# Performance work log

Measured on AMD Instinct MI355X. Metric: run time of the kernel, lower is better.

Reference implementation:

```python
import jax, jax.numpy as jnp
import numpy as np

NUM_HEADS = 16
BASE = 10000.0


def setup_inputs() -> dict:
    key = jax.random.key(0)
    ks = jax.random.split(key, 5)
    b, n, c = 4, 4096, 1024
    return {
        "x": jax.random.normal(ks[0], (b, n, c), jnp.float32),
        "W_qk": jax.random.normal(ks[1], (2 * c, c), jnp.float32) * 0.02,
        "b_qk": jax.random.normal(ks[2], (2 * c,), jnp.float32) * 0.02,
        "lepe_w": jax.random.normal(ks[3], (c, 1, 3), jnp.float32) * 0.1,
        "lepe_b": jax.random.normal(ks[4], (c,), jnp.float32) * 0.02,
    }


def _rope(t, cos_t, sin_t):
    # t: (b, n, c); pairs rotated by per-pair angle theta_k (constant over positions,
    # faithful to the original module's RoPE which has no position dependence)
    k_max = t.shape[-1] // 2
    tr = t.reshape(*t.shape[:-1], k_max, 2)
    x0, x1 = tr[..., 0], tr[..., 1]
    out = jnp.stack([cos_t * x0 - sin_t * x1, sin_t * x0 + cos_t * x1], axis=-1)
    return out.reshape(t.shape)


def reference(x, W_qk, b_qk, lepe_w, lepe_b):
    b, n, c = x.shape
    h = NUM_HEADS
    d = c // h
    k_max = c // 2
    theta = 1.0 / (BASE ** (jnp.arange(k_max, dtype=jnp.float32) / k_max))
    cos_t, sin_t = jnp.cos(theta), jnp.sin(theta)

    qk = x @ W_qk.T + b_qk                      # (b, n, 2c)
    q = jax.nn.elu(qk[..., :c]) + 1.0           # (b, n, c)
    k = jax.nn.elu(qk[..., c:]) + 1.0

    q_rope = _rope(q, cos_t, sin_t).reshape(b, n, h, d).transpose(0, 2, 1, 3)
    k_rope = _rope(k, cos_t, sin_t).reshape(b, n, h, d).transpose(0, 2, 1, 3)
    qh = q.reshape(b, n, h, d).transpose(0, 2, 1, 3)
    kh = k.reshape(b, n, h, d).transpose(0, 2, 1, 3)
    vh = x.reshape(b, n, h, d).transpose(0, 2, 1, 3)

    # z normalization: q . mean_n(k)
    z = 1.0 / (jnp.einsum("bhnd,bhd->bhn", qh, kh.mean(axis=2)) + 1e-6)  # (b,h,n)

    # kv accumulation: (k_rope / sqrt(n))^T @ (v / sqrt(n))  -> (b,h,d,d)
    kv = jnp.einsum("bhnd,bhne->bhde", k_rope, vh) * (1.0 / n)
    attn = jnp.einsum("bhnd,bhde->bhne", q_rope, kv) * z[..., None]  # (b,h,n,d)
    out = attn.transpose(0, 2, 1, 3).reshape(b, n, c)

    # depthwise conv positional term on v (== x, since v is x reshaped back)
    v_cn = x.transpose(0, 2, 1)  # (b, c, n)
    pe = jax.lax.conv_general_dilated(
        v_cn, lepe_w, window_strides=(1,), padding=((1, 1),),
        feature_group_count=c, dimension_numbers=("NCH", "OIH", "NCH"))
    pe = pe + lepe_b[None, :, None]
    return out + pe.transpose(0, 2, 1)
```

## Files before the change

### kernel.cpp

```cpp
#include <hip/hip_runtime.h>
#include <hip/hip_bf16.h>
#include <math.h>

typedef unsigned short u16;
typedef __attribute__((ext_vector_type(8))) short s16x8;
typedef __attribute__((ext_vector_type(4))) float f32x4;

#define B_ 4
#define N_ 4096
#define C_ 1024
#define M_ (B_*N_)
#define NT_ 16

__device__ __forceinline__ u16 f2bf(float f) {
  unsigned u = __builtin_bit_cast(unsigned, f);
  u = u + 0x7fffu + ((u >> 16) & 1u);
  return (u16)(u >> 16);
}
__device__ __forceinline__ float bf2f(u16 h) {
  unsigned u = ((unsigned)h) << 16;
  return __builtin_bit_cast(float, u);
}

__global__ void trig_kernel(float* __restrict__ ctab, float* __restrict__ stab) {
  const int i = threadIdx.x;
  const float theta = powf(10000.f, -(float)i * (1.f/512.f));
  ctab[i] = cosf(theta);
  stab[i] = sinf(theta);
}

__global__ __launch_bounds__(256) void cast_kernel(
    const float* __restrict__ x, const float* __restrict__ w,
    u16* __restrict__ xb, u16* __restrict__ wb)
{
  const int NX4 = M_*C_/4;
  const int NW4 = 2048*C_/4;
  int tid = blockIdx.x*256 + threadIdx.x;
  int stride = gridDim.x*256;
  for (int i = tid; i < NX4; i += stride) {
    f32x4 v = ((const f32x4*)x)[i];
    ushort4 o;
    o.x = f2bf(v[0]); o.y = f2bf(v[1]); o.z = f2bf(v[2]); o.w = f2bf(v[3]);
    ((ushort4*)xb)[i] = o;
  }
  for (int i = tid; i < NW4; i += stride) {
    f32x4 v = ((const f32x4*)w)[i];
    ushort4 o;
    o.x = f2bf(v[0]); o.y = f2bf(v[1]); o.z = f2bf(v[2]); o.w = f2bf(v[3]);
    ((ushort4*)wb)[i] = o;
  }
}

__global__ __launch_bounds__(512, 2) void gemm_kernel(
    const u16* __restrict__ xb, const u16* __restrict__ wb,
    const float* __restrict__ bqk,
    const float* __restrict__ ctab, const float* __restrict__ stab,
    u16* __restrict__ qrb, u16* __restrict__ krb)
{
  __shared__ __align__(16) unsigned char SH[131072];
  unsigned char (*As)[32768] = (unsigned char (*)[32768])SH;
  unsigned char (*Bs)[32768] = (unsigned char (*)[32768])(SH + 65536);
  const int t = threadIdx.x;
  const int l = t & 63;
  const int w = t >> 6;
  const int wm = w >> 2, wn = w & 3;
  const int m0 = blockIdx.x * 256;
  const int n0 = blockIdx.y * 256;

  f32x4 acc[8][4];
  #pragma unroll
  for (int a = 0; a < 8; ++a)
    #pragma unroll
    for (int b = 0; b < 4; ++b) acc[a][b] = (f32x4){0.f,0.f,0.f,0.f};

  const int s_cole = ((t & 7) ^ ((t >> 3) & 7)) << 3;
  const size_t a_base = (size_t)(m0 + (t >> 3)) * 1024 + s_cole;
  const size_t b_base = (size_t)(n0 + (t >> 3)) * 1024 + s_cole;

  #define GLA(buf, kt, i_)                                                     \
    __builtin_amdgcn_global_load_lds(                                          \
      (const __attribute__((address_space(1))) void*)(xb + a_base + (size_t)(i_)*65536 + (kt)*64), \
      (__attribute__((address_space(3))) void*)(&As[buf][((i_)*512 + w*64)*16]), 16, 0, 0)
  #define GLB(buf, kt, i_)                                                     \
    __builtin_amdgcn_global_load_lds(                                          \
      (const __attribute__((address_space(1))) void*)(wb + b_base + (size_t)(i_)*65536 + (kt)*64), \
      (__attribute__((address_space(3))) void*)(&Bs[buf][((i_)*512 + w*64)*16]), 16, 0, 0)

  GLA(0,0,0); GLA(0,0,1); GLA(0,0,2); GLA(0,0,3);
  GLB(0,0,0); GLB(0,0,1); GLB(0,0,2); GLB(0,0,3);
  asm volatile("s_waitcnt vmcnt(0)" ::: "memory");
  __builtin_amdgcn_s_barrier();

  for (int kt = 0; kt < NT_; ++kt) {
    const int cur = kt & 1;
    const int nx = cur ^ 1;
    const unsigned char* Ab = As[cur];
    const unsigned char* Bb = Bs[cur];
    s16x8 bfr[4][2];
    #pragma unroll
    for (int p = 0; p < 4; ++p) {
      s16x8 af[2][2];
      #pragma unroll
      for (int f = 0; f < 2; ++f) {
        const int r = wm*128 + (2*p + f)*16 + (l & 15);
        #pragma unroll
        for (int ks = 0; ks < 2; ++ks) {
          const int kbyte = ks*64 + ((l >> 4) << 4);
          af[f][ks] = *(const s16x8*)(Ab + r*128 + (kbyte ^ ((r & 7) << 4)));
        }
      }
      if (p == 0) {
        #pragma unroll
        for (int nf = 0; nf < 4; ++nf) {
          const int r = wn*64 + nf*16 + (l & 15);
          #pragma unroll
          for (int ks = 0; ks < 2; ++ks) {
            const int kbyte = ks*64 + ((l >> 4) << 4);
            bfr[nf][ks] = *(const s16x8*)(Bb + r*128 + (kbyte ^ ((r & 7) << 4)));
          }
        }
      }
      if (kt + 1 < NT_) {
        if (p == 0) { GLB(nx, kt+1, 0); GLB(nx, kt+1, 1); GLB(nx, kt+1, 2); GLB(nx, kt+1, 3); }
        if (p == 1) { GLA(nx, kt+1, 0); GLA(nx, kt+1, 2); }
        if (p == 2) { GLA(nx, kt+1, 1); GLA(nx, kt+1, 3); }
      }
      __builtin_amdgcn_s_barrier();
      __builtin_amdgcn_s_setprio(1);
      #pragma unroll
      for (int f = 0; f < 2; ++f)
        #pragma unroll
        for (int nf = 0; nf < 4; ++nf)
          #pragma unroll
          for (int ks = 0; ks < 2; ++ks)
            acc[2*p + f][nf] = __builtin_amdgcn_mfma_f32_16x16x32_bf16(
                af[f][ks], bfr[nf][ks], acc[2*p + f][nf], 0, 0, 0);
      __builtin_amdgcn_s_setprio(0);
      if (p == 1) {
        if (kt < NT_ - 1) asm volatile("s_waitcnt vmcnt(6)" ::: "memory");
        else              asm volatile("s_waitcnt vmcnt(0)" ::: "memory");
      }
      if (p == 3 && kt + 1 < NT_) {
        asm volatile("s_waitcnt vmcnt(2)" ::: "memory");
      }
      __builtin_amdgcn_s_barrier();
    }
  }
  #undef GLA
  #undef GLB

  #pragma unroll
  for (int nf = 0; nf < 4; ++nf) {
    const int lcol = wn*64 + nf*16 + (l & 15);
    const int col = n0 + lcol;
    const float bias = bqk[col];
    const int cc = col & 1023;
    const float cn = ctab[cc >> 1];
    const float sn = stab[cc >> 1];
    const int lcolp2 = (lcol & ~1) * 2;
    #pragma unroll
    for (int mf = 0; mf < 8; ++mf) {
      #pragma unroll
      for (int j = 0; j < 4; ++j) {
        const int rloc = wm*128 + mf*16 + ((l >> 4) << 2) + j;
        float v = acc[mf][nf][j] + bias;
        v = (v > 0.f) ? (v + 1.f) : __expf(v);
        const float vp = __shfl_xor(v, 1);
        if (((l & 1) == 0) == (mf < 4)) {
          const float e = (l & 1) ? vp : v;
          const float o = (l & 1) ? v : vp;
          const unsigned pack = (unsigned)f2bf(cn*e - sn*o)
                              | ((unsigned)f2bf(sn*e + cn*o) << 16);
          *(unsigned*)(SH + rloc*512 + (lcolp2 ^ ((rloc & 7) << 4))) = pack;
        }
      }
    }
  }
  __syncthreads();
  {
    u16* dst = (n0 < 1024) ? qrb : krb;
    const int colbase = n0 & 1023;
    #pragma unroll
    for (int it = 0; it < 16; ++it) {
      const int chunk = it*512 + t;
      const int r = chunk >> 5;
      const int c = chunk & 31;
      const s16x8 val = *(const s16x8*)(SH + r*512 + ((c ^ (r & 7)) << 4));
      *(s16x8*)(dst + (size_t)(m0 + r)*1024 + colbase + c*8) = val;
    }
  }
}

__global__ __launch_bounds__(256, 4) void kvpart_kernel(
    const u16* __restrict__ krb, const u16* __restrict__ xb,
    float* __restrict__ partial, float* __restrict__ ksump)
{
  __shared__ float red[2][64][65];
  __shared__ float ksred[4][64];
  const int t = threadIdx.x;
  const int l = t & 63;
  const int nsub = t >> 6;
  const int dg = l >> 3, eg = l & 7;
  const int d0 = dg*8, e0 = eg*8;
  const int blk = blockIdx.x;
  const int bh = blk >> 4;
  const int ns = blk & 15;
  const int b = bh >> 4, h = bh & 15;

  float acc[8][8];
  #pragma unroll
  for (int i=0;i<8;++i)
    #pragma unroll
    for (int j=0;j<8;++j) acc[i][j]=0.f;
  float ksum[8];
  #pragma unroll
  for (int i=0;i<8;++i) ksum[i]=0.f;

  const size_t base = ((size_t)b*4096 + ns*256 + nsub*64) * 1024 + h*64;
  #pragma unroll 2
  for (int it = 0; it < 64; ++it) {
    const size_t roff = base + (size_t)it*1024;
    const s16x8 k8 = *(const s16x8*)(krb + roff + d0);
    const s16x8 v8 = *(const s16x8*)(xb + roff + e0);
    float kf[8], vf[8];
    #pragma unroll
    for (int i=0;i<8;++i){ kf[i]=bf2f((u16)k8[i]); vf[i]=bf2f((u16)v8[i]); }
    #pragma unroll
    for (int i=0;i<8;++i){
      ksum[i]+=kf[i];
      #pragma unroll
      for (int j=0;j<8;++j) acc[i][j] += kf[i]*vf[j];
    }
  }

  if (eg == 0) {
    #pragma unroll
    for (int i=0;i<8;++i) ksred[nsub][d0+i] = ksum[i];
  }
  if (nsub >= 2) {
    #pragma unroll
    for (int i=0;i<8;++i)
      #pragma unroll
      for (int j=0;j<8;++j) red[nsub-2][l][i*8+j] = acc[i][j];
  }
  __syncthreads();
  if (t < 64) {
    const float s4 = ksred[0][t]+ksred[1][t]+ksred[2][t]+ksred[3][t];
    ksump[((size_t)ns*64 + bh)*64 + t] = s4;
  }
  if (nsub < 2) {
    #pragma unroll
    for (int i=0;i<8;++i)
      #pragma unroll
      for (int j=0;j<8;++j) acc[i][j] += red[nsub][l][i*8+j];
  }
  __syncthreads();
  if (nsub == 1) {
    #pragma unroll
    for (int i=0;i<8;++i)
      #pragma unroll
      for (int j=0;j<8;++j) red[0][l][i*8+j] = acc[i][j];
  }
  __syncthreads();
  if (nsub == 0) {
    float* dst = partial + ((size_t)ns*64 + bh)*4096 + d0*64 + e0;
    #pragma unroll
    for (int i=0;i<8;++i) {
      f32x4 lo, hi;
      #pragma unroll
      for (int j=0;j<4;++j) { lo[j] = acc[i][j] + red[0][l][i*8+j];
                              hi[j] = acc[i][j+4] + red[0][l][i*8+j+4]; }
      *(f32x4*)(dst + i*64)     = lo;
      *(f32x4*)(dst + i*64 + 4) = hi;
    }
  }
}

__global__ __launch_bounds__(256) void kvred_kernel(
    const float* __restrict__ partial, const float* __restrict__ ksump,
    u16* __restrict__ kvbT, float* __restrict__ kmr)
{
  __shared__ float s[4096];
  const int bh = blockIdx.x;
  const int t = threadIdx.x;
  const float inv_n = 1.f / 4096.f;
  f32x4 a0={0,0,0,0}, a1={0,0,0,0}, a2={0,0,0,0}, a3={0,0,0,0};
  #pragma unroll
  for (int sl=0; sl<16; ++sl) {
    const f32x4* p = (const f32x4*)(partial + ((size_t)sl*64 + bh)*4096 + t*16);
    a0 += p[0]; a1 += p[1]; a2 += p[2]; a3 += p[3];
  }
  ((f32x4*)s)[t*4+0]=a0; ((f32x4*)s)[t*4+1]=a1;
  ((f32x4*)s)[t*4+2]=a2; ((f32x4*)s)[t*4+3]=a3;
  if (t < 64) {
    float ks = 0.f;
    #pragma unroll
    for (int sl = 0; sl < 16; ++sl) ks += ksump[((size_t)sl*64 + bh)*64 + t];
    kmr[bh*64 + t] = ks * inv_n;
  }
  __syncthreads();
  s16x8 o0, o1;
  #pragma unroll
  for (int j=0;j<8;++j) {
    o0[j] = (short)f2bf(s[((t&3)*16 + j)*64 + (t>>2)] * inv_n);
    o1[j] = (short)f2bf(s[((t&3)*16 + 8 + j)*64 + (t>>2)] * inv_n);
  }
  *(s16x8*)(kvbT + (size_t)bh*4096 + t*16) = o0;
  *(s16x8*)(kvbT + (size_t)bh*4096 + t*16 + 8) = o1;
}

__global__ __launch_bounds__(256) void attn_kernel(
    const u16* __restrict__ qrb, const u16* __restrict__ kvbT,
    const float* __restrict__ kmr, const u16* __restrict__ xb,
    const float* __restrict__ lw, const float* __restrict__ lb,
    float* __restrict__ out)
{
  __shared__ __align__(16) unsigned char As[16384];
  __shared__ __align__(16) unsigned char Bs[8192];
  __shared__ float lws[192], lbs[64];
  __shared__ float kms[64];
  __shared__ float zs[128];
  const int t = threadIdx.x, l = t & 63, w = t >> 6;
  const int m0 = blockIdx.x * 128;
  const int h = blockIdx.y, b = blockIdx.z;
  const size_t qbase = ((size_t)b*4096 + m0) * 1024 + h*64;
  const u16* kvsrc = kvbT + ((size_t)(b*16 + h) << 12);

  #pragma unroll
  for (int i = 0; i < 4; ++i) {
    const int jc   = i*256 + t;
    const int row  = jc >> 3;
    const int cole = (((jc & 7) << 4) ^ ((row & 7) << 4)) >> 1;
    const int ldsoff = (i*256 + w*64) * 16;
    __builtin_amdgcn_global_load_lds(
      (const __attribute__((address_space(1))) void*)(qrb + qbase + (size_t)row*1024 + cole),
      (__attribute__((address_space(3))) void*)(As + ldsoff), 16, 0, 0);
  }
  #pragma unroll
  for (int i = 0; i < 2; ++i) {
    const int jc   = i*256 + t;
    const int row  = jc >> 3;
    const int cole = (((jc & 7) << 4) ^ ((row & 7) << 4)) >> 1;
    const int ldsoff = (i*256 + w*64) * 16;
    __builtin_amdgcn_global_load_lds(
      (const __attribute__((address_space(1))) void*)(kvsrc + (size_t)row*64 + cole),
      (__attribute__((address_space(3))) void*)(Bs + ldsoff), 16, 0, 0);
  }
  if (t < 192) lws[t] = lw[h*192 + t];
  if (t >= 192)  lbs[t-192] = lb[h*64 + (t-192)];
  if (t < 64) kms[t] = kmr[(b*16 + h)*64 + t];
  __syncthreads();

  {
    const int r = t >> 1, half = t & 1;
    const int swz = (r & 7) << 4;
    float zp = 0.f;
    #pragma unroll
    for (int c = 0; c < 4; ++c) {
      const int kb = half*64 + c*16;
      const s16x8 qv = *(const s16x8*)(As + r*128 + (kb ^ swz));
      #pragma unroll
      for (int j = 0; j < 8; ++j) zp += bf2f((u16)qv[j]) * kms[half*32 + c*8 + j];
    }
    zp += __shfl_xor(zp, 1);
    if (!half) zs[r] = 1.f / (zp + 1e-6f);
  }

  f32x4 acc[2][4];
  #pragma unroll
  for (int a = 0; a < 2; ++a)
    #pragma unroll
    for (int c = 0; c < 4; ++c) acc[a][c] = (f32x4){0.f,0.f,0.f,0.f};

  #pragma unroll
  for (int ks = 0; ks < 2; ++ks) {
    const int kbyte = ks*64 + ((l >> 4) << 4);
    s16x8 af[2], bf[4];
    #pragma unroll
    for (int mi = 0; mi < 2; ++mi) {
      const int r = w*32 + mi*16 + (l & 15);
      af[mi] = *(const s16x8*)(As + r*128 + (kbyte ^ ((r & 7) << 4)));
    }
    #pragma unroll
    for (int ni = 0; ni < 4; ++ni) {
      const int r = ni*16 + (l & 15);
      bf[ni] = *(const s16x8*)(Bs + r*128 + (kbyte ^ ((r & 7) << 4)));
    }
    #pragma unroll
    for (int mi = 0; mi < 2; ++mi)
      #pragma unroll
      for (int ni = 0; ni < 4; ++ni)
        acc[mi][ni] = __builtin_amdgcn_mfma_f32_16x16x32_bf16(af[mi], bf[ni], acc[mi][ni], 0, 0, 0);
  }
  __syncthreads();

  #pragma unroll
  for (int mi = 0; mi < 2; ++mi) {
    #pragma unroll
    for (int j = 0; j < 4; ++j) {
      const int rowm = m0 + w*32 + mi*16 + ((l >> 4) << 2) + j;
      const float zr = zs[rowm - m0];
      const size_t rbase = ((size_t)b*4096 + rowm)*1024;
      #pragma unroll
      for (int ni = 0; ni < 4; ++ni) {
        const int cl = ni*16 + (l & 15);
        const int c = h*64 + cl;
        float pe = lbs[cl] + bf2f(xb[rbase + c])*lws[cl*3+1];
        if (rowm > 0)    pe += bf2f(xb[rbase - 1024 + c])*lws[cl*3];
        if (rowm < 4095) pe += bf2f(xb[rbase + 1024 + c])*lws[cl*3+2];
        out[rbase + c] = acc[mi][ni][j]*zr + pe;
      }
    }
  }
}

extern "C" void kernel_launch(void* const* d_in, const int* in_sizes, int n_in,
                              void* d_out, int out_size, void* d_ws, size_t ws_size,
                              hipStream_t stream) {
  const float* x   = (const float*)d_in[0];
  const float* Wqk = (const float*)d_in[1];
  const float* bqk = (const float*)d_in[2];
  const float* lw  = (const float*)d_in[3];
  const float* lb  = (const float*)d_in[4];
  float* out = (float*)d_out;

  char* ws = (char*)d_ws;
  u16* xb    = (u16*)(ws);
  u16* qrb   = (u16*)(ws + 33554432ull);
  u16* krb   = (u16*)(ws + 67108864ull);
  u16* wb    = (u16*)(ws + 100663296ull);
  float* kmr = (float*)(ws + 104857600ull);
  float* ctab= (float*)(ws + 104874368ull);
  float* stab= (float*)(ws + 104876416ull);
  u16* kvbT  = (u16*)(ws + 104878464ull);
  float* partial = out;
  float* ksump   = out + 4194304;

  hipLaunchKernelGGL(trig_kernel, dim3(1), dim3(512), 0, stream, ctab, stab);
  hipLaunchKernelGGL(cast_kernel, dim3(2048), dim3(256), 0, stream, x, Wqk, xb, wb);
  hipLaunchKernelGGL(gemm_kernel, dim3(64, 8), dim3(512), 0, stream, xb, wb, bqk, ctab, stab, qrb, krb);
  hipLaunchKernelGGL(kvpart_kernel, dim3(1024), dim3(256), 0, stream, krb, xb, partial, ksump);
  hipLaunchKernelGGL(kvred_kernel, dim3(64), dim3(256), 0, stream, partial, ksump, kvbT, kmr);
  hipLaunchKernelGGL(attn_kernel, dim3(32, 16, 4), dim3(256), 0, stream, qrb, kvbT, kmr, xb, lw, lb, out);
}
```

Measured before the change: 209.8 us.

## Restructure GEMM k-loop into two half-tile phases with fewer barriers

Measured after the change: 205.8 us. Within noise of the previous version (-1.9%).

```diff
diff --git a/kernel.cpp b/kernel.cpp
--- a/kernel.cpp
+++ b/kernel.cpp
@@ -86,9 +86,10 @@
       (const __attribute__((address_space(1))) void*)(wb + b_base + (size_t)(i_)*65536 + (kt)*64), \
       (__attribute__((address_space(3))) void*)(&Bs[buf][((i_)*512 + w*64)*16]), 16, 0, 0)
 
-  GLA(0,0,0); GLA(0,0,1); GLA(0,0,2); GLA(0,0,3);
   GLB(0,0,0); GLB(0,0,1); GLB(0,0,2); GLB(0,0,3);
-  asm volatile("s_waitcnt vmcnt(0)" ::: "memory");
+  GLA(0,0,0); GLA(0,0,2);
+  GLA(0,0,1); GLA(0,0,3);
+  asm volatile("s_waitcnt vmcnt(2)" ::: "memory");
   __builtin_amdgcn_s_barrier();
 
   for (int kt = 0; kt < NT_; ++kt) {
@@ -96,55 +97,74 @@
     const int nx = cur ^ 1;
     const unsigned char* Ab = As[cur];
     const unsigned char* Bb = Bs[cur];
+
+    if (kt + 1 < NT_) {
+      GLB(nx, kt+1, 0); GLB(nx, kt+1, 1); GLB(nx, kt+1, 2); GLB(nx, kt+1, 3);
+      GLA(nx, kt+1, 0); GLA(nx, kt+1, 2);
+    }
     s16x8 bfr[4][2];
     #pragma unroll
-    for (int p = 0; p < 4; ++p) {
-      s16x8 af[2][2];
-      #pragma unroll
-      for (int f = 0; f < 2; ++f) {
-        const int r = wm*128 + (2*p + f)*16 + (l & 15);
+    for (int nf = 0; nf < 4; ++nf) {
+      const int r = wn*64 + nf*16 + (l & 15);
+      #pragma unroll
+      for (int ks = 0; ks < 2; ++ks) {
+        const int kbyte = ks*64 + ((l >> 4) << 4);
+        bfr[nf][ks] = *(const s16x8*)(Bb + r*128 + (kbyte ^ ((r & 7) << 4)));
+      }
+    }
+    {
+      s16x8 af[4][2];
+      #pragma unroll
+      for (int f = 0; f < 4; ++f) {
+        const int r = wm*128 + f*16 + (l & 15);
         #pragma unroll
         for (int ks = 0; ks < 2; ++ks) {
           const int kbyte = ks*64 + ((l >> 4) << 4);
           af[f][ks] = *(const s16x8*)(Ab + r*128 + (kbyte ^ ((r & 7) << 4)));
         }
       }
-      if (p == 0) {
-        #pragma unroll
-        for (int nf = 0; nf < 4; ++nf) {
-          const int r = wn*64 + nf*16 + (l & 15);
-          #pragma unroll
-          for (int ks = 0; ks < 2; ++ks) {
-            const int kbyte = ks*64 + ((l >> 4) << 4);
-            bfr[nf][ks] = *(const s16x8*)(Bb + r*128 + (kbyte ^ ((r & 7) << 4)));
-          }
-        }
-      }
-      if (kt + 1 < NT_) {
-        if (p == 0) { GLB(nx, kt+1, 0); GLB(nx, kt+1, 1); GLB(nx, kt+1, 2); GLB(nx, kt+1, 3); }
-        if (p == 1) { GLA(nx, kt+1, 0); GLA(nx, kt+1, 2); }
-        if (p == 2) { GLA(nx, kt+1, 1); GLA(nx, kt+1, 3); }
-      }
-      __builtin_amdgcn_s_barrier();
       __builtin_amdgcn_s_setprio(1);
       #pragma unroll
-      for (int f = 0; f < 2; ++f)
+      for (int f = 0; f < 4; ++f)
         #pragma unroll
         for (int nf = 0; nf < 4; ++nf)
           #pragma unroll
           for (int ks = 0; ks < 2; ++ks)
-            acc[2*p + f][nf] = __builtin_amdgcn_mfma_f32_16x16x32_bf16(
-                af[f][ks], bfr[nf][ks], acc[2*p + f][nf], 0, 0, 0);
+            acc[f][nf] = __builtin_amdgcn_mfma_f32_16x16x32_bf16(
+                af[f][ks], bfr[nf][ks], acc[f][nf], 0, 0, 0);
       __builtin_amdgcn_s_setprio(0);
-      if (p == 1) {
-        if (kt < NT_ - 1) asm volatile("s_waitcnt vmcnt(6)" ::: "memory");
-        else              asm volatile("s_waitcnt vmcnt(0)" ::: "memory");
+    }
+    if (kt + 1 < NT_) asm volatile("s_waitcnt vmcnt(6)" ::: "memory");
+    else              asm volatile("s_waitcnt vmcnt(0)" ::: "memory");
+    __builtin_amdgcn_s_barrier();
+
+    if (kt + 1 < NT_) {
+      GLA(nx, kt+1, 1); GLA(nx, kt+1, 3);
+    }
+    {
+      s16x8 af[4][2];
+      #pragma unroll
+      for (int f = 0; f < 4; ++f) {
+        const int r = wm*128 + (f + 4)*16 + (l & 15);
+        #pragma unroll
+        for (int ks = 0; ks < 2; ++ks) {
+          const int kbyte = ks*64 + ((l >> 4) << 4);
+          af[f][ks] = *(const s16x8*)(Ab + r*128 + (kbyte ^ ((r & 7) << 4)));
+        }
       }
-      if (p == 3 && kt + 1 < NT_) {
-        asm volatile("s_waitcnt vmcnt(2)" ::: "memory");
-      }
-      __builtin_amdgcn_s_barrier();
-    }
+      __builtin_amdgcn_s_setprio(1);
+      #pragma unroll
+      for (int f = 0; f < 4; ++f)
+        #pragma unroll
+        for (int nf = 0; nf < 4; ++nf)
+          #pragma unroll
+          for (int ks = 0; ks < 2; ++ks)
+            acc[f + 4][nf] = __builtin_amdgcn_mfma_f32_16x16x32_bf16(
+                af[f][ks], bfr[nf][ks], acc[f + 4][nf], 0, 0, 0);
+      __builtin_amdgcn_s_setprio(0);
+    }
+    if (kt + 1 < NT_) asm volatile("s_waitcnt vmcnt(2)" ::: "memory");
+    __builtin_amdgcn_s_barrier();
   }
   #undef GLA
   #undef GLB
```
